# Optimization experiments

Measured on AMD Instinct MI355X. Metric: run time of the kernel, lower is better.

## Reference

```python
import jax, jax.numpy as jnp
import numpy as np

B, C, H, W = 2, 256, 64, 64
HEADS, DIM_HEAD = 8, 64
INNER = HEADS * DIM_HEAD


def setup_inputs() -> dict:
    key = jax.random.key(0)
    k1, k2, k3, k4 = jax.random.split(key, 4)
    x = jax.random.normal(k1, (B, C, H, W), dtype=jnp.float32)
    # 1x1 conv weights stored as [out_ch, in_ch]
    w_qkv = jax.random.normal(k2, (3 * INNER, C), dtype=jnp.float32) * (1.0 / np.sqrt(C))
    w_out = jax.random.normal(k3, (C, INNER), dtype=jnp.float32) * (1.0 / np.sqrt(INNER))
    b_out = jax.random.normal(k4, (C,), dtype=jnp.float32) * 0.01
    return {"x": x, "w_qkv": w_qkv, "w_out": w_out, "b_out": b_out}


def reference(x, w_qkv, w_out, b_out):
    b, c, h, w = x.shape
    n = h * w
    # 1x1 conv == channel matmul
    qkv = jnp.einsum('oc,bchw->bohw', w_qkv, x)  # [B, 3*inner, H, W]
    qkv = qkv.reshape(b, 3, HEADS, DIM_HEAD, n)
    qkv = jnp.transpose(qkv, (1, 0, 2, 4, 3))    # [3, B, heads, N, dim_head]
    q, k, v = qkv[0], qkv[1], qkv[2]
    scale = 1.0 / (DIM_HEAD ** 0.5)
    dots = jnp.einsum('bhnd,bhmd->bhnm', q, k) * scale  # [B, heads, N, N]
    attn = jax.nn.softmax(dots, axis=-1)
    out = jnp.einsum('bhnm,bhmd->bhnd', attn, v)        # [B, heads, N, dim_head]
    out = jnp.transpose(out, (0, 1, 3, 2)).reshape(b, INNER, h, w)
    return jnp.einsum('ci,bihw->bchw', w_out, out) + b_out[None, :, None, None]
```

## Files before the change

kernel.cpp:

```cpp
#include <hip/hip_runtime.h>
#include <hip/hip_bf16.h>

typedef unsigned short u16;
typedef __attribute__((ext_vector_type(8))) short bf16x8;
typedef __attribute__((ext_vector_type(4))) float f32x4;
typedef __attribute__((ext_vector_type(8))) unsigned short u16x8;
typedef __attribute__((ext_vector_type(4))) unsigned short u16x4;

#define N_POS 4096
#define HEADS 8
#define DHEAD 64
#define CIN   256
#define INNER 512
#define NSPLIT 2
#define JCHUNK (N_POS / NSPLIT)

__device__ __forceinline__ u16 f2bf(float f) {
    union { float f; unsigned int u; } v; v.f = f;
    unsigned int u = v.u + 0x7FFFu + ((v.u >> 16) & 1u);
    return (u16)(u >> 16);
}

__device__ __forceinline__ float b2f(u16 x) {
    union { float f; unsigned int u; } v;
    v.u = ((unsigned int)x) << 16;
    return v.f;
}

__device__ __forceinline__ unsigned int pkbf2(float lo, float hi) {
    union { __hip_bfloat162 b; unsigned int u; } cv;
    cv.b = __float22bfloat162_rn(make_float2(lo, hi));
    return cv.u;
}

__global__ __launch_bounds__(256) void k0_prep(const float* __restrict__ x,
                                               const float* __restrict__ w_qkv,
                                               const float* __restrict__ w_out,
                                               u16* __restrict__ xT,
                                               u16* __restrict__ wq,
                                               u16* __restrict__ wo) {
    int bid = blockIdx.x;
    int t   = threadIdx.x;
    if (bid < 256) {
        int b = bid >> 7, rest = bid & 127;
        int n  = (rest & 15) * 256 + t;
        int c0 = (rest >> 4) * 32;
        const float* xp = x + (size_t)b * CIN * N_POS + n;
        u16* op = xT + ((size_t)(b * N_POS + n)) * CIN + c0;
        for (int g = 0; g < 4; ++g) {
            u16x8 v;
            for (int j = 0; j < 8; ++j)
                v[j] = f2bf(xp[(size_t)(c0 + g * 8 + j) * N_POS]);
            *(u16x8*)(op + g * 8) = v;
        }
    } else if (bid < 448) {
        size_t idx = (size_t)(bid - 256) * 2048 + t * 8;
        u16x8 v;
        for (int j = 0; j < 8; ++j) v[j] = f2bf(w_qkv[idx + j]);
        *(u16x8*)(wq + idx) = v;
    } else {
        size_t idx = (size_t)(bid - 448) * 2048 + t * 8;
        u16x8 v;
        for (int j = 0; j < 8; ++j) v[j] = f2bf(w_out[idx + j]);
        *(u16x8*)(wo + idx) = v;
    }
}

__global__ __launch_bounds__(256, 4) void k1_qkv(const u16* __restrict__ wq,
                                                 const u16* __restrict__ xT,
                                                 u16* __restrict__ q_ws,
                                                 u16* __restrict__ k_ws,
                                                 u16* __restrict__ vt_ws) {
    __shared__ u16 Alds[64 * 72];
    __shared__ u16 Blds[128 * 72];
    int tid = threadIdx.x;
    int n0  = blockIdx.x * 128;
    int by  = blockIdx.y;
    int b   = blockIdx.z;
    int o0  = by * 64;
    int sel = by >> 3;
    int h   = by & 7;
    int wv = tid >> 6, l = tid & 63, quad = l >> 4, l15 = l & 15;
    int arow = tid >> 2, aseg = (tid & 3) * 16;
    int brow = tid >> 1, bseg = (tid & 1) * 32;

    f32x4 acc[8] = {};
    for (int c0 = 0; c0 < CIN; c0 += 64) {
        const u16* wp = wq + (size_t)(o0 + arow) * CIN + c0 + aseg;
        *(u16x8*)&Alds[arow * 72 + aseg]     = *(const u16x8*)wp;
        *(u16x8*)&Alds[arow * 72 + aseg + 8] = *(const u16x8*)(wp + 8);
        const u16* xp = xT + ((size_t)(b * N_POS + n0 + brow)) * CIN + c0 + bseg;
        for (int g = 0; g < 4; ++g)
            *(u16x8*)&Blds[brow * 72 + bseg + g * 8] = *(const u16x8*)(xp + g * 8);
        __syncthreads();
        bf16x8 af0 = *(const bf16x8*)&Alds[(wv * 16 + l15) * 72 + quad * 8];
        bf16x8 af1 = *(const bf16x8*)&Alds[(wv * 16 + l15) * 72 + 32 + quad * 8];
        for (int nt = 0; nt < 8; ++nt) {
            const u16* bb = &Blds[(nt * 16 + l15) * 72 + quad * 8];
            acc[nt] = __builtin_amdgcn_mfma_f32_16x16x32_bf16(af0, *(const bf16x8*)bb, acc[nt], 0, 0, 0);
            acc[nt] = __builtin_amdgcn_mfma_f32_16x16x32_bf16(af1, *(const bf16x8*)(bb + 32), acc[nt], 0, 0, 0);
        }
        __syncthreads();
    }
    const float QSCALE = 0.125f * 1.44269504088896f;
    float sc = (sel == 0) ? QSCALE : 1.0f;
    int dbase = wv * 16 + quad * 4;
    for (int nt = 0; nt < 8; ++nt) {
        int n = n0 + nt * 16 + l15;
        if (sel < 2) {
            u16* base = (sel == 0) ? q_ws : k_ws;
            u16x4 pk;
            for (int r = 0; r < 4; ++r) pk[r] = f2bf(acc[nt][r] * sc);
            *(u16x4*)&base[((size_t)((b * HEADS + h) * N_POS + n)) * DHEAD + dbase] = pk;
        } else {
            for (int r = 0; r < 4; ++r)
                vt_ws[((size_t)((b * HEADS + h) * DHEAD + dbase + r)) * N_POS + n] =
                    f2bf(acc[nt][r]);
        }
    }
}

__global__ __launch_bounds__(256, 4) void k2_attn(const u16* __restrict__ q_ws,
                                                  const u16* __restrict__ k_ws,
                                                  const u16* __restrict__ vt_ws,
                                                  u16* __restrict__ op_ws,
                                                  float* __restrict__ lw_ws) {
    __shared__ u16 Klds[64 * 72];
    __shared__ u16 Vlds[64 * 72];
    int tid = threadIdx.x;
    int q0  = blockIdx.x * 128;
    int bh  = blockIdx.y;
    int half = blockIdx.z;
    int jbase = half * JCHUNK;
    int wv = tid >> 6, l = tid & 63, quad = l >> 4, l15 = l & 15;
    int srow = tid >> 2, sseg = tid & 3;
    int srowp = (srow & 0x23) | ((srow & 4) << 2) | ((srow & 0x18) >> 1);

    const u16* qp = q_ws + ((size_t)(bh * N_POS + q0 + wv * 32 + l15)) * DHEAD + quad * 8;
    bf16x8 bq[2][2];
    for (int it = 0; it < 2; ++it) {
        bq[it][0] = *(const bf16x8*)(qp + (size_t)it * 16 * DHEAD);
        bq[it][1] = *(const bf16x8*)(qp + (size_t)it * 16 * DHEAD + 32);
    }

    f32x4 Oacc[2][4] = {};
    float lsum[2] = {0.f, 0.f};

    const u16* kp = k_ws + ((size_t)(bh * N_POS + srow)) * DHEAD + sseg * 16;
    const u16* vp = vt_ws + ((size_t)(bh * DHEAD + srow)) * N_POS + sseg * 16;

    u16x8 pf0 = *(const u16x8*)(kp + (size_t)jbase * DHEAD);
    u16x8 pf1 = *(const u16x8*)(kp + (size_t)jbase * DHEAD + 8);
    u16x8 pf2 = *(const u16x8*)(vp + jbase);
    u16x8 pf3 = *(const u16x8*)(vp + jbase + 8);

    for (int j0 = jbase; j0 < jbase + JCHUNK; j0 += 64) {
        *(u16x8*)&Klds[srowp * 72 + sseg * 16]     = pf0;
        *(u16x8*)&Klds[srowp * 72 + sseg * 16 + 8] = pf1;
        *(u16x8*)&Vlds[srow * 72 + sseg * 16]      = pf2;
        *(u16x8*)&Vlds[srow * 72 + sseg * 16 + 8]  = pf3;
        __syncthreads();

        if (j0 + 64 < jbase + JCHUNK) {
            const u16* kpj = kp + (size_t)(j0 + 64) * DHEAD;
            pf0 = *(const u16x8*)kpj;
            pf1 = *(const u16x8*)(kpj + 8);
            pf2 = *(const u16x8*)(vp + j0 + 64);
            pf3 = *(const u16x8*)(vp + j0 + 72);
        }

        unsigned int pkw[2][2][4];
        for (int p = 0; p < 2; ++p)
            for (int a = 0; a < 2; ++a) {
                const u16* kb = &Klds[((2 * p + a) * 16 + l15) * 72 + quad * 8];
                bf16x8 kf0 = *(const bf16x8*)kb;
                bf16x8 kf1 = *(const bf16x8*)(kb + 32);
                f32x4 z[2];
                for (int it = 0; it < 2; ++it) {
                    f32x4 t = {};
                    t = __builtin_amdgcn_mfma_f32_16x16x32_bf16(kf0, bq[it][0], t, 0, 0, 0);
                    t = __builtin_amdgcn_mfma_f32_16x16x32_bf16(kf1, bq[it][1], t, 0, 0, 0);
                    z[it] = t;
                }
                for (int it = 0; it < 2; ++it) {
                    float e0 = __builtin_amdgcn_exp2f(z[it][0]);
                    float e1 = __builtin_amdgcn_exp2f(z[it][1]);
                    float e2 = __builtin_amdgcn_exp2f(z[it][2]);
                    float e3 = __builtin_amdgcn_exp2f(z[it][3]);
                    lsum[it] += (e0 + e1) + (e2 + e3);
                    pkw[it][p][2 * a]     = pkbf2(e0, e1);
                    pkw[it][p][2 * a + 1] = pkbf2(e2, e3);
                }
            }

        for (int dt = 0; dt < 4; ++dt)
            for (int p = 0; p < 2; ++p) {
                bf16x8 vf = *(const bf16x8*)&Vlds[(dt * 16 + l15) * 72 + p * 32 + quad * 8];
                for (int it = 0; it < 2; ++it) {
                    union { unsigned int u[4]; bf16x8 v; } cv;
                    cv.u[0] = pkw[it][p][0]; cv.u[1] = pkw[it][p][1];
                    cv.u[2] = pkw[it][p][2]; cv.u[3] = pkw[it][p][3];
                    Oacc[it][dt] = __builtin_amdgcn_mfma_f32_16x16x32_bf16(vf, cv.v, Oacc[it][dt], 0, 0, 0);
                }
            }
        __syncthreads();
    }

    int b = bh >> 3, h = bh & 7;
    u16* opb   = op_ws + (size_t)half * 2 * N_POS * INNER;
    float* lwb = lw_ws + (size_t)half * 2 * HEADS * N_POS;
    for (int it = 0; it < 2; ++it) {
        float ls = lsum[it];
        ls += __shfl_xor(ls, 16);
        ls += __shfl_xor(ls, 32);
        int n = q0 + wv * 32 + it * 16 + l15;
        if (quad == 0) lwb[(size_t)bh * N_POS + n] = ls;
        u16* dst = opb + ((size_t)(b * N_POS + n)) * INNER + h * DHEAD;
        for (int dt = 0; dt < 4; ++dt) {
            u16x4 w;
            for (int r = 0; r < 4; ++r) w[r] = f2bf(Oacc[it][dt][r]);
            *(u16x4*)&dst[dt * 16 + quad * 4] = w;
        }
    }
}

__global__ __launch_bounds__(256, 2) void k3_out(const u16* __restrict__ wo,
                                                 const float* __restrict__ b_out,
                                                 const u16* __restrict__ op_ws,
                                                 const float* __restrict__ lw_ws,
                                                 float* __restrict__ out) {
    __shared__ u16 Alds[64 * 136];
    __shared__ u16 Blds[64 * 136];
    int tid = threadIdx.x;
    int n0 = blockIdx.x * 64;
    int c0 = blockIdx.y * 64;
    int b  = blockIdx.z;
    int wv = tid >> 6, l = tid & 63, quad = l >> 4, l15 = l & 15;
    int srow = tid >> 2, sseg = (tid & 3) * 32;

    f32x4 acc[4] = {};
    for (int i0 = 0; i0 < INNER; i0 += 128) {
        const u16* wp = wo + (size_t)(c0 + srow) * INNER + i0 + sseg;
        for (int g = 0; g < 4; ++g)
            *(u16x8*)&Alds[srow * 136 + sseg + g * 8] = *(const u16x8*)(wp + g * 8);
        {
            int i = i0 + sseg;
            int h = i >> 6;
            int n = n0 + srow;
            size_t lidx = ((size_t)(b * HEADS + h)) * N_POS + n;
            float ls = 0.f;
            for (int s = 0; s < NSPLIT; ++s)
                ls += lw_ws[(size_t)s * 2 * HEADS * N_POS + lidx];
            float inv = 1.0f / ls;
            const u16* p = op_ws + ((size_t)(b * N_POS + n)) * INNER + i;
            for (int g = 0; g < 4; ++g) {
                float a8[8] = {};
                for (int s = 0; s < NSPLIT; ++s) {
                    u16x8 v = *(const u16x8*)(p + (size_t)s * 2 * N_POS * INNER + g * 8);
                    for (int k = 0; k < 8; ++k) a8[k] += b2f(v[k]);
                }
                u16x8 o;
                for (int k = 0; k < 8; ++k) o[k] = f2bf(a8[k] * inv);
                *(u16x8*)&Blds[srow * 136 + sseg + g * 8] = o;
            }
        }
        __syncthreads();
        for (int kc = 0; kc < 4; ++kc) {
            bf16x8 af = *(const bf16x8*)&Alds[(wv * 16 + l15) * 136 + kc * 32 + quad * 8];
            for (int nt = 0; nt < 4; ++nt) {
                bf16x8 bfrag = *(const bf16x8*)&Blds[(nt * 16 + l15) * 136 + kc * 32 + quad * 8];
                acc[nt] = __builtin_amdgcn_mfma_f32_16x16x32_bf16(af, bfrag, acc[nt], 0, 0, 0);
            }
        }
        __syncthreads();
    }
    for (int r = 0; r < 4; ++r) {
        int c = c0 + wv * 16 + quad * 4 + r;
        float bias = b_out[c];
        for (int nt = 0; nt < 4; ++nt) {
            int n = n0 + nt * 16 + l15;
            out[((size_t)(b * CIN + c)) * N_POS + n] = acc[nt][r] + bias;
        }
    }
}

extern "C" void kernel_launch(void* const* d_in, const int* in_sizes, int n_in,
                              void* d_out, int out_size, void* d_ws, size_t ws_size,
                              hipStream_t stream) {
    const float* x     = (const float*)d_in[0];
    const float* w_qkv = (const float*)d_in[1];
    const float* w_out = (const float*)d_in[2];
    const float* b_out = (const float*)d_in[3];
    float* out = (float*)d_out;

    u16* ws    = (u16*)d_ws;
    u16* xT    = ws;
    u16* q_ws  = xT   + (size_t)2 * N_POS * CIN;
    u16* k_ws  = q_ws + (size_t)2 * HEADS * N_POS * DHEAD;
    u16* vt_ws = k_ws + (size_t)2 * HEADS * N_POS * DHEAD;
    u16* wq_bf = vt_ws + (size_t)2 * HEADS * N_POS * DHEAD;
    u16* wo_bf = wq_bf + (size_t)3 * INNER * CIN;
    u16* op_ws = wo_bf + (size_t)CIN * INNER;
    float* lw_ws = (float*)(op_ws + (size_t)NSPLIT * 2 * N_POS * INNER);

    hipLaunchKernelGGL(k0_prep, dim3(512), dim3(256), 0, stream,
                       x, w_qkv, w_out, xT, wq_bf, wo_bf);
    hipLaunchKernelGGL(k1_qkv, dim3(32, 24, 2), dim3(256), 0, stream,
                       wq_bf, xT, q_ws, k_ws, vt_ws);
    hipLaunchKernelGGL(k2_attn, dim3(32, 16, NSPLIT), dim3(256), 0, stream,
                       q_ws, k_ws, vt_ws, op_ws, lw_ws);
    hipLaunchKernelGGL(k3_out, dim3(64, 4, 2), dim3(256), 0, stream,
                       wo_bf, b_out, op_ws, lw_ws, out);
}
```

Measured before the change: 178.7 us.

## Fuse fp32-to-bf16 prep into QKV and output GEMMs; stage QKV stores through LDS

Removes the separate prep kernel. The QKV projection now reads fp32 x and w_qkv directly, converting and transposing them while loading LDS tiles, and the output projection converts fp32 w_out on the fly. This avoids one launch and the write-then-read round trip of the bf16 intermediates. The QKV epilogue also stages results through LDS so that global stores of q/k and the transposed v are coalesced 16-byte writes. In exchange, each k1 block repeatedly reads fp32 data, twice the bytes of bf16, and repeats the conversion work across blocks.

```diff
diff --git a/kernel.cpp b/kernel.cpp
--- a/kernel.cpp
+++ b/kernel.cpp
@@ -33,41 +33,8 @@
     return cv.u;
 }
 
-__global__ __launch_bounds__(256) void k0_prep(const float* __restrict__ x,
-                                               const float* __restrict__ w_qkv,
-                                               const float* __restrict__ w_out,
-                                               u16* __restrict__ xT,
-                                               u16* __restrict__ wq,
-                                               u16* __restrict__ wo) {
-    int bid = blockIdx.x;
-    int t   = threadIdx.x;
-    if (bid < 256) {
-        int b = bid >> 7, rest = bid & 127;
-        int n  = (rest & 15) * 256 + t;
-        int c0 = (rest >> 4) * 32;
-        const float* xp = x + (size_t)b * CIN * N_POS + n;
-        u16* op = xT + ((size_t)(b * N_POS + n)) * CIN + c0;
-        for (int g = 0; g < 4; ++g) {
-            u16x8 v;
-            for (int j = 0; j < 8; ++j)
-                v[j] = f2bf(xp[(size_t)(c0 + g * 8 + j) * N_POS]);
-            *(u16x8*)(op + g * 8) = v;
-        }
-    } else if (bid < 448) {
-        size_t idx = (size_t)(bid - 256) * 2048 + t * 8;
-        u16x8 v;
-        for (int j = 0; j < 8; ++j) v[j] = f2bf(w_qkv[idx + j]);
-        *(u16x8*)(wq + idx) = v;
-    } else {
-        size_t idx = (size_t)(bid - 448) * 2048 + t * 8;
-        u16x8 v;
-        for (int j = 0; j < 8; ++j) v[j] = f2bf(w_out[idx + j]);
-        *(u16x8*)(wo + idx) = v;
-    }
-}
-
-__global__ __launch_bounds__(256, 4) void k1_qkv(const u16* __restrict__ wq,
-                                                 const u16* __restrict__ xT,
+__global__ __launch_bounds__(256, 4) void k1_qkv(const float* __restrict__ w_qkv,
+                                                 const float* __restrict__ x,
                                                  u16* __restrict__ q_ws,
                                                  u16* __restrict__ k_ws,
                                                  u16* __restrict__ vt_ws) {
@@ -80,18 +47,29 @@
     int o0  = by * 64;
     int sel = by >> 3;
     int h   = by & 7;
+    int bh  = b * HEADS + h;
     int wv = tid >> 6, l = tid & 63, quad = l >> 4, l15 = l & 15;
     int arow = tid >> 2, aseg = (tid & 3) * 16;
-    int brow = tid >> 1, bseg = (tid & 1) * 32;
+    int tn = tid & 127, tcg = (tid >> 7) * 32;
 
     f32x4 acc[8] = {};
     for (int c0 = 0; c0 < CIN; c0 += 64) {
-        const u16* wp = wq + (size_t)(o0 + arow) * CIN + c0 + aseg;
-        *(u16x8*)&Alds[arow * 72 + aseg]     = *(const u16x8*)wp;
-        *(u16x8*)&Alds[arow * 72 + aseg + 8] = *(const u16x8*)(wp + 8);
-        const u16* xp = xT + ((size_t)(b * N_POS + n0 + brow)) * CIN + c0 + bseg;
-        for (int g = 0; g < 4; ++g)
-            *(u16x8*)&Blds[brow * 72 + bseg + g * 8] = *(const u16x8*)(xp + g * 8);
+        {
+            const float* wp = w_qkv + (size_t)(o0 + arow) * CIN + c0 + aseg;
+            u16x8 v0, v1;
+            for (int k = 0; k < 8; ++k) { v0[k] = f2bf(wp[k]); v1[k] = f2bf(wp[8 + k]); }
+            *(u16x8*)&Alds[arow * 72 + aseg]     = v0;
+            *(u16x8*)&Alds[arow * 72 + aseg + 8] = v1;
+        }
+        {
+            const float* xp = x + ((size_t)b * CIN + c0 + tcg) * N_POS + n0 + tn;
+            for (int j = 0; j < 4; ++j) {
+                u16x8 v;
+                for (int k = 0; k < 8; ++k)
+                    v[k] = f2bf(xp[(size_t)(j * 8 + k) * N_POS]);
+                *(u16x8*)&Blds[tn * 72 + tcg + j * 8] = v;
+            }
+        }
         __syncthreads();
         bf16x8 af0 = *(const bf16x8*)&Alds[(wv * 16 + l15) * 72 + quad * 8];
         bf16x8 af1 = *(const bf16x8*)&Alds[(wv * 16 + l15) * 72 + 32 + quad * 8];
@@ -102,20 +80,34 @@
         }
         __syncthreads();
     }
+
     const float QSCALE = 0.125f * 1.44269504088896f;
-    float sc = (sel == 0) ? QSCALE : 1.0f;
     int dbase = wv * 16 + quad * 4;
-    for (int nt = 0; nt < 8; ++nt) {
-        int n = n0 + nt * 16 + l15;
-        if (sel < 2) {
-            u16* base = (sel == 0) ? q_ws : k_ws;
-            u16x4 pk;
-            for (int r = 0; r < 4; ++r) pk[r] = f2bf(acc[nt][r] * sc);
-            *(u16x4*)&base[((size_t)((b * HEADS + h) * N_POS + n)) * DHEAD + dbase] = pk;
-        } else {
+    if (sel < 2) {
+        float sc = (sel == 0) ? QSCALE : 1.0f;
+        for (int nt = 0; nt < 8; ++nt) {
+            u16x4 w;
+            for (int r = 0; r < 4; ++r) w[r] = f2bf(acc[nt][r] * sc);
+            *(u16x4*)&Blds[(nt * 16 + l15) * 72 + dbase] = w;
+        }
+        __syncthreads();
+        u16* base = (sel == 0) ? q_ws : k_ws;
+        u16* dst = base + ((size_t)bh * N_POS + n0) * DHEAD;
+        for (int pass = 0; pass < 4; ++pass) {
+            int flat = pass * 2048 + tid * 8;
+            int row = flat >> 6, d = flat & 63;
+            *(u16x8*)&dst[flat] = *(const u16x8*)&Blds[row * 72 + d];
+        }
+    } else {
+        for (int nt = 0; nt < 8; ++nt)
             for (int r = 0; r < 4; ++r)
-                vt_ws[((size_t)((b * HEADS + h) * DHEAD + dbase + r)) * N_POS + n] =
-                    f2bf(acc[nt][r]);
+                Blds[(dbase + r) * 136 + nt * 16 + l15] = f2bf(acc[nt][r]);
+        __syncthreads();
+        u16* dst = vt_ws + (size_t)bh * DHEAD * N_POS + n0;
+        for (int pass = 0; pass < 4; ++pass) {
+            int d = pass * 16 + (tid >> 4);
+            int nseg = (tid & 15) * 8;
+            *(u16x8*)&dst[(size_t)d * N_POS + nseg] = *(const u16x8*)&Blds[d * 136 + nseg];
         }
     }
 }
@@ -224,7 +216,7 @@
     }
 }
 
-__global__ __launch_bounds__(256, 2) void k3_out(const u16* __restrict__ wo,
+__global__ __launch_bounds__(256, 2) void k3_out(const float* __restrict__ w_out,
                                                  const float* __restrict__ b_out,
                                                  const u16* __restrict__ op_ws,
                                                  const float* __restrict__ lw_ws,
@@ -240,9 +232,14 @@
 
     f32x4 acc[4] = {};
     for (int i0 = 0; i0 < INNER; i0 += 128) {
-        const u16* wp = wo + (size_t)(c0 + srow) * INNER + i0 + sseg;
-        for (int g = 0; g < 4; ++g)
-            *(u16x8*)&Alds[srow * 136 + sseg + g * 8] = *(const u16x8*)(wp + g * 8);
+        {
+            const float* wp = w_out + (size_t)(c0 + srow) * INNER + i0 + sseg;
+            for (int g = 0; g < 4; ++g) {
+                u16x8 o;
+                for (int k = 0; k < 8; ++k) o[k] = f2bf(wp[g * 8 + k]);
+                *(u16x8*)&Alds[srow * 136 + sseg + g * 8] = o;
+            }
+        }
         {
             int i = i0 + sseg;
             int h = i >> 6;
@@ -294,21 +291,16 @@
     float* out = (float*)d_out;
 
     u16* ws    = (u16*)d_ws;
-    u16* xT    = ws;
-    u16* q_ws  = xT   + (size_t)2 * N_POS * CIN;
+    u16* q_ws  = ws;
     u16* k_ws  = q_ws + (size_t)2 * HEADS * N_POS * DHEAD;
     u16* vt_ws = k_ws + (size_t)2 * HEADS * N_POS * DHEAD;
-    u16* wq_bf = vt_ws + (size_t)2 * HEADS * N_POS * DHEAD;
-    u16* wo_bf = wq_bf + (size_t)3 * INNER * CIN;
-    u16* op_ws = wo_bf + (size_t)CIN * INNER;
+    u16* op_ws = vt_ws + (size_t)2 * HEADS * N_POS * DHEAD;
     float* lw_ws = (float*)(op_ws + (size_t)NSPLIT * 2 * N_POS * INNER);
 
-    hipLaunchKernelGGL(k0_prep, dim3(512), dim3(256), 0, stream,
-                       x, w_qkv, w_out, xT, wq_bf, wo_bf);
     hipLaunchKernelGGL(k1_qkv, dim3(32, 24, 2), dim3(256), 0, stream,
-                       wq_bf, xT, q_ws, k_ws, vt_ws);
+                       w_qkv, x, q_ws, k_ws, vt_ws);
     hipLaunchKernelGGL(k2_attn, dim3(32, 16, NSPLIT), dim3(256), 0, stream,
                        q_ws, k_ws, vt_ws, op_ws, lw_ws);
     hipLaunchKernelGGL(k3_out, dim3(64, 4, 2), dim3(256), 0, stream,
-                       wo_bf, b_out, op_ws, lw_ws, out);
-}
+                       w_out, b_out, op_ws, lw_ws, out);
+}
```

Result: slower. 182.9 us (+2.3%).

## Enlarge attention query tile, split keys three ways, coalesce QKV stores via LDS

Applied to the files above, without the earlier changes.

The attention kernel now gives each block 256 queries (64 per wave) instead of 128, so each K/V tile loaded into shared memory serves twice as many queries. The key range is split into three uneven chunks instead of two, and the inner loop interleaves exp and PV work per key sub-block, which keeps register pressure down. Launch bounds are relaxed to 3 blocks per SM to make room for the larger accumulators. Separately, the QKV projection epilogue stages its results through shared memory so the global stores to Q, K and transposed V are wide and coalesced rather than scattered. The costs are higher register use, lower occupancy, fewer blocks in the grid, and a dependence on the output kernel handling three partial splits.

```diff
diff --git a/kernel.cpp b/kernel.cpp
--- a/kernel.cpp
+++ b/kernel.cpp
@@ -12,8 +12,9 @@
 #define DHEAD 64
 #define CIN   256
 #define INNER 512
-#define NSPLIT 2
-#define JCHUNK (N_POS / NSPLIT)
+#define NSPLIT 3
+#define JBEG(s) ((s) * 1344 + ((s) ? 64 : 0))
+#define JEND(s) ((s) * 1344 + 1408)
 
 __device__ __forceinline__ u16 f2bf(float f) {
     union { float f; unsigned int u; } v; v.f = f;
@@ -80,6 +81,7 @@
     int o0  = by * 64;
     int sel = by >> 3;
     int h   = by & 7;
+    int bh  = b * HEADS + h;
     int wv = tid >> 6, l = tid & 63, quad = l >> 4, l15 = l & 15;
     int arow = tid >> 2, aseg = (tid & 3) * 16;
     int brow = tid >> 1, bseg = (tid & 1) * 32;
@@ -102,25 +104,39 @@
         }
         __syncthreads();
     }
+
     const float QSCALE = 0.125f * 1.44269504088896f;
-    float sc = (sel == 0) ? QSCALE : 1.0f;
     int dbase = wv * 16 + quad * 4;
-    for (int nt = 0; nt < 8; ++nt) {
-        int n = n0 + nt * 16 + l15;
-        if (sel < 2) {
-            u16* base = (sel == 0) ? q_ws : k_ws;
-            u16x4 pk;
-            for (int r = 0; r < 4; ++r) pk[r] = f2bf(acc[nt][r] * sc);
-            *(u16x4*)&base[((size_t)((b * HEADS + h) * N_POS + n)) * DHEAD + dbase] = pk;
-        } else {
+    if (sel < 2) {
+        float sc = (sel == 0) ? QSCALE : 1.0f;
+        for (int nt = 0; nt < 8; ++nt) {
+            u16x4 w;
+            for (int r = 0; r < 4; ++r) w[r] = f2bf(acc[nt][r] * sc);
+            *(u16x4*)&Blds[(nt * 16 + l15) * 72 + dbase] = w;
+        }
+        __syncthreads();
+        u16* base = (sel == 0) ? q_ws : k_ws;
+        u16* dst = base + ((size_t)bh * N_POS + n0) * DHEAD;
+        for (int pass = 0; pass < 4; ++pass) {
+            int flat = pass * 2048 + tid * 8;
+            int row = flat >> 6, d = flat & 63;
+            *(u16x8*)&dst[flat] = *(const u16x8*)&Blds[row * 72 + d];
+        }
+    } else {
+        for (int nt = 0; nt < 8; ++nt)
             for (int r = 0; r < 4; ++r)
-                vt_ws[((size_t)((b * HEADS + h) * DHEAD + dbase + r)) * N_POS + n] =
-                    f2bf(acc[nt][r]);
-        }
-    }
-}
-
-__global__ __launch_bounds__(256, 4) void k2_attn(const u16* __restrict__ q_ws,
+                Blds[(dbase + r) * 136 + nt * 16 + l15] = f2bf(acc[nt][r]);
+        __syncthreads();
+        u16* dst = vt_ws + (size_t)bh * DHEAD * N_POS + n0;
+        for (int pass = 0; pass < 4; ++pass) {
+            int d = pass * 16 + (tid >> 4);
+            int nseg = (tid & 15) * 8;
+            *(u16x8*)&dst[(size_t)d * N_POS + nseg] = *(const u16x8*)&Blds[d * 136 + nseg];
+        }
+    }
+}
+
+__global__ __launch_bounds__(256, 3) void k2_attn(const u16* __restrict__ q_ws,
                                                   const u16* __restrict__ k_ws,
                                                   const u16* __restrict__ vt_ws,
                                                   u16* __restrict__ op_ws,
@@ -128,40 +144,40 @@
     __shared__ u16 Klds[64 * 72];
     __shared__ u16 Vlds[64 * 72];
     int tid = threadIdx.x;
-    int q0  = blockIdx.x * 128;
+    int q0  = blockIdx.x * 256;
     int bh  = blockIdx.y;
     int half = blockIdx.z;
-    int jbase = half * JCHUNK;
+    int jbeg = JBEG(half), jend = JEND(half);
     int wv = tid >> 6, l = tid & 63, quad = l >> 4, l15 = l & 15;
     int srow = tid >> 2, sseg = tid & 3;
     int srowp = (srow & 0x23) | ((srow & 4) << 2) | ((srow & 0x18) >> 1);
 
-    const u16* qp = q_ws + ((size_t)(bh * N_POS + q0 + wv * 32 + l15)) * DHEAD + quad * 8;
-    bf16x8 bq[2][2];
-    for (int it = 0; it < 2; ++it) {
+    const u16* qp = q_ws + ((size_t)(bh * N_POS + q0 + wv * 64 + l15)) * DHEAD + quad * 8;
+    bf16x8 bq[4][2];
+    for (int it = 0; it < 4; ++it) {
         bq[it][0] = *(const bf16x8*)(qp + (size_t)it * 16 * DHEAD);
         bq[it][1] = *(const bf16x8*)(qp + (size_t)it * 16 * DHEAD + 32);
     }
 
-    f32x4 Oacc[2][4] = {};
-    float lsum[2] = {0.f, 0.f};
+    f32x4 Oacc[4][4] = {};
+    float lsum[4] = {0.f, 0.f, 0.f, 0.f};
 
     const u16* kp = k_ws + ((size_t)(bh * N_POS + srow)) * DHEAD + sseg * 16;
     const u16* vp = vt_ws + ((size_t)(bh * DHEAD + srow)) * N_POS + sseg * 16;
 
-    u16x8 pf0 = *(const u16x8*)(kp + (size_t)jbase * DHEAD);
-    u16x8 pf1 = *(const u16x8*)(kp + (size_t)jbase * DHEAD + 8);
-    u16x8 pf2 = *(const u16x8*)(vp + jbase);
-    u16x8 pf3 = *(const u16x8*)(vp + jbase + 8);
-
-    for (int j0 = jbase; j0 < jbase + JCHUNK; j0 += 64) {
+    u16x8 pf0 = *(const u16x8*)(kp + (size_t)jbeg * DHEAD);
+    u16x8 pf1 = *(const u16x8*)(kp + (size_t)jbeg * DHEAD + 8);
+    u16x8 pf2 = *(const u16x8*)(vp + jbeg);
+    u16x8 pf3 = *(const u16x8*)(vp + jbeg + 8);
+
+    for (int j0 = jbeg; j0 < jend; j0 += 64) {
         *(u16x8*)&Klds[srowp * 72 + sseg * 16]     = pf0;
         *(u16x8*)&Klds[srowp * 72 + sseg * 16 + 8] = pf1;
         *(u16x8*)&Vlds[srow * 72 + sseg * 16]      = pf2;
         *(u16x8*)&Vlds[srow * 72 + sseg * 16 + 8]  = pf3;
         __syncthreads();
 
-        if (j0 + 64 < jbase + JCHUNK) {
+        if (j0 + 64 < jend) {
             const u16* kpj = kp + (size_t)(j0 + 64) * DHEAD;
             pf0 = *(const u16x8*)kpj;
             pf1 = *(const u16x8*)(kpj + 8);
@@ -169,51 +185,46 @@
             pf3 = *(const u16x8*)(vp + j0 + 72);
         }
 
-        unsigned int pkw[2][2][4];
-        for (int p = 0; p < 2; ++p)
+        for (int p = 0; p < 2; ++p) {
+            unsigned int pkw[4][4];
             for (int a = 0; a < 2; ++a) {
                 const u16* kb = &Klds[((2 * p + a) * 16 + l15) * 72 + quad * 8];
                 bf16x8 kf0 = *(const bf16x8*)kb;
                 bf16x8 kf1 = *(const bf16x8*)(kb + 32);
-                f32x4 z[2];
-                for (int it = 0; it < 2; ++it) {
+                for (int it = 0; it < 4; ++it) {
                     f32x4 t = {};
                     t = __builtin_amdgcn_mfma_f32_16x16x32_bf16(kf0, bq[it][0], t, 0, 0, 0);
                     t = __builtin_amdgcn_mfma_f32_16x16x32_bf16(kf1, bq[it][1], t, 0, 0, 0);
-                    z[it] = t;
-                }
-                for (int it = 0; it < 2; ++it) {
-                    float e0 = __builtin_amdgcn_exp2f(z[it][0]);
-                    float e1 = __builtin_amdgcn_exp2f(z[it][1]);
-                    float e2 = __builtin_amdgcn_exp2f(z[it][2]);
-                    float e3 = __builtin_amdgcn_exp2f(z[it][3]);
+                    float e0 = __builtin_amdgcn_exp2f(t[0]);
+                    float e1 = __builtin_amdgcn_exp2f(t[1]);
+                    float e2 = __builtin_amdgcn_exp2f(t[2]);
+                    float e3 = __builtin_amdgcn_exp2f(t[3]);
                     lsum[it] += (e0 + e1) + (e2 + e3);
-                    pkw[it][p][2 * a]     = pkbf2(e0, e1);
-                    pkw[it][p][2 * a + 1] = pkbf2(e2, e3);
+                    pkw[it][2 * a]     = pkbf2(e0, e1);
+                    pkw[it][2 * a + 1] = pkbf2(e2, e3);
                 }
             }
-
-        for (int dt = 0; dt < 4; ++dt)
-            for (int p = 0; p < 2; ++p) {
+            for (int dt = 0; dt < 4; ++dt) {
                 bf16x8 vf = *(const bf16x8*)&Vlds[(dt * 16 + l15) * 72 + p * 32 + quad * 8];
-                for (int it = 0; it < 2; ++it) {
+                for (int it = 0; it < 4; ++it) {
                     union { unsigned int u[4]; bf16x8 v; } cv;
-                    cv.u[0] = pkw[it][p][0]; cv.u[1] = pkw[it][p][1];
-                    cv.u[2] = pkw[it][p][2]; cv.u[3] = pkw[it][p][3];
+                    cv.u[0] = pkw[it][0]; cv.u[1] = pkw[it][1];
+                    cv.u[2] = pkw[it][2]; cv.u[3] = pkw[it][3];
                     Oacc[it][dt] = __builtin_amdgcn_mfma_f32_16x16x32_bf16(vf, cv.v, Oacc[it][dt], 0, 0, 0);
                 }
             }
+        }
         __syncthreads();
     }
 
     int b = bh >> 3, h = bh & 7;
     u16* opb   = op_ws + (size_t)half * 2 * N_POS * INNER;
     float* lwb = lw_ws + (size_t)half * 2 * HEADS * N_POS;
-    for (int it = 0; it < 2; ++it) {
+    for (int it = 0; it < 4; ++it) {
         float ls = lsum[it];
         ls += __shfl_xor(ls, 16);
         ls += __shfl_xor(ls, 32);
-        int n = q0 + wv * 32 + it * 16 + l15;
+        int n = q0 + wv * 64 + it * 16 + l15;
         if (quad == 0) lwb[(size_t)bh * N_POS + n] = ls;
         u16* dst = opb + ((size_t)(b * N_POS + n)) * INNER + h * DHEAD;
         for (int dt = 0; dt < 4; ++dt) {
@@ -307,7 +318,7 @@
                        x, w_qkv, w_out, xT, wq_bf, wo_bf);
     hipLaunchKernelGGL(k1_qkv, dim3(32, 24, 2), dim3(256), 0, stream,
                        wq_bf, xT, q_ws, k_ws, vt_ws);
-    hipLaunchKernelGGL(k2_attn, dim3(32, 16, NSPLIT), dim3(256), 0, stream,
+    hipLaunchKernelGGL(k2_attn, dim3(16, 16, NSPLIT), dim3(256), 0, stream,
                        q_ws, k_ws, vt_ws, op_ws, lw_ws);
     hipLaunchKernelGGL(k3_out, dim3(64, 4, 2), dim3(256), 0, stream,
                        wo_bf, b_out, op_ws, lw_ws, out);
```

Result: slower. 391.5 us (+119.0%).
